# Optimization experiments

Hardware: AMD Instinct MI355X
Metric: run time of the kernel (lower is better)

Reference implementation:

```python
import jax, jax.numpy as jnp
import numpy as np
from jax import lax

B, C, H, W, K = 32, 128, 56, 56, 5
CR = C // 4          # reduced channels in weight-gen MLP
CE = 4 * C           # expanded channels
EPS = 1e-6


def setup_inputs() -> dict:
    key = jax.random.key(0)
    ks = jax.random.split(key, 8)
    s = lambda fan: 1.0 / np.sqrt(fan)
    return {
        "x": jax.random.normal(ks[0], (B, C, H, W), jnp.float32),
        "w_fc1": jax.random.normal(ks[1], (CR, C), jnp.float32) * s(C),
        "ln1_w": jnp.ones((CR,), jnp.float32),
        "ln1_b": jnp.zeros((CR,), jnp.float32),
        "w_fc2": jax.random.normal(ks[2], (C * K * K, CR), jnp.float32) * s(CR),
        "ln2_w": jnp.ones((C,), jnp.float32),
        "ln2_b": jnp.zeros((C,), jnp.float32),
        "w_expand": jax.random.normal(ks[3], (CE, C), jnp.float32) * s(C),
        "w_shrink": jax.random.normal(ks[4], (C, CE), jnp.float32) * s(CE),
        "grn_gamma": jax.random.normal(ks[5], (CE,), jnp.float32) * 0.1,
        "grn_beta": jax.random.normal(ks[6], (CE,), jnp.float32) * 0.1,
    }


def _ln(v, w, b, axis):
    u = v.mean(axis, keepdims=True)
    s2 = jnp.square(v - u).mean(axis, keepdims=True)
    return (v - u) * lax.rsqrt(s2 + EPS) * w + b


def reference(x, w_fc1, ln1_w, ln1_b, w_fc2, ln2_w, ln2_b, w_expand, w_shrink,
              grn_gamma, grn_beta):
    b, c, h, w = x.shape
    # ---- dynamic weight generation: pool -> fc1 -> LN -> fc2 ----
    pooled = x.mean((2, 3))                                  # [B, C]
    hdn = pooled @ w_fc1.T                                   # [B, CR]
    hdn = _ln(hdn, ln1_w, ln1_b, axis=-1)                    # channels_first LN over CR
    dyn = hdn @ w_fc2.T                                      # [B, C*K*K]
    dyn_w = dyn.reshape(b * c, 1, K, K)                      # per-sample depthwise kernels
    # ---- per-sample dynamic depthwise conv (groups = B*C) ----
    pad = K // 2
    out = lax.conv_general_dilated(
        x.reshape(1, b * c, h, w), dyn_w,
        window_strides=(1, 1), padding=[(pad, pad), (pad, pad)],
        dimension_numbers=("NCHW", "OIHW", "NCHW"),
        feature_group_count=b * c,
    ).reshape(b, c, h, w)
    # ---- LN (channels_first) over channel dim ----
    u = out.mean(1, keepdims=True)
    s2 = jnp.square(out - u).mean(1, keepdims=True)
    out = (out - u) * lax.rsqrt(s2 + EPS)
    out = ln2_w[None, :, None, None] * out + ln2_b[None, :, None, None]
    # ---- expand 1x1 -> GELU -> GRN -> shrink 1x1 ----
    out = jnp.einsum("bchw,oc->bohw", out, w_expand)         # [B, 4C, H, W]
    out = jax.nn.gelu(out, approximate=False)
    gx = jnp.sqrt(jnp.sum(jnp.square(out), axis=(2, 3), keepdims=True))  # [B,4C,1,1]
    nx = gx / (gx.mean(1, keepdims=True) + EPS)
    g = grn_gamma[None, :, None, None]
    bt = grn_beta[None, :, None, None]
    out = g * (out * nx) + bt + out
    out = jnp.einsum("bohw,co->bchw", out, w_shrink)         # [B, C, H, W]
    return out + x
```

## Files before the change

kernel.cpp:

```cpp
#include <hip/hip_runtime.h>
#include <hip/hip_bf16.h>

#define B_   32
#define C_   128
#define H_   56
#define W_   56
#define HW_  (H_*W_)
#define BHW_ (B_*HW_)
#define K5_  5
#define KK_  25
#define CR_  32
#define CE_  512
#define EPS_ 1e-6f

typedef __hip_bfloat16 bf16;
typedef __attribute__((ext_vector_type(8))) short short8;
typedef __attribute__((ext_vector_type(4))) float f32x4;


__device__ __forceinline__ float wave_reduce_sum(float v) {
#pragma unroll
  for (int off = 32; off > 0; off >>= 1) v += __shfl_down(v, off, 64);
  return v;
}
__device__ __forceinline__ float bf2f(unsigned short u) {
  return __uint_as_float(((unsigned)u) << 16);
}
__device__ __forceinline__ unsigned short f2bf_bits(float f) {
  bf16 h = __float2bfloat16(f);
  unsigned short u;
  __builtin_memcpy(&u, &h, 2);
  return u;
}
__device__ __forceinline__ float fast_gelu(float v) {
  float t = __expf(-1.702f * v);
  return v * __builtin_amdgcn_rcpf(1.0f + t);
}

__global__ __launch_bounds__(256) void prep_kernel(const float* __restrict__ we,
                                                   const float* __restrict__ ws,
                                                   bf16* __restrict__ weB,
                                                   bf16* __restrict__ wsB) {
  int i = blockIdx.x * 256 + threadIdx.x;
  if (i < CE_ * C_) {
    weB[i] = __float2bfloat16(we[i]);
    wsB[i] = __float2bfloat16(ws[i]);
  }
}

__global__ __launch_bounds__(256) void pool_kernel(const float* __restrict__ x,
                                                   float* __restrict__ pooled) {
  int bc = blockIdx.x;
  const float* xp = x + (size_t)bc * HW_;
  float s = 0.f;
  for (int i = threadIdx.x; i < HW_; i += 256) s += xp[i];
  s = wave_reduce_sum(s);
  __shared__ float red[4];
  int lane = threadIdx.x & 63, wid = threadIdx.x >> 6;
  if (lane == 0) red[wid] = s;
  __syncthreads();
  if (threadIdx.x == 0) pooled[bc] = (red[0] + red[1] + red[2] + red[3]) * (1.0f / HW_);
}

__global__ __launch_bounds__(256) void fc_kernel(const float* __restrict__ pooled,
                                                 const float* __restrict__ w_fc1,
                                                 const float* __restrict__ ln1_w,
                                                 const float* __restrict__ ln1_b,
                                                 const float* __restrict__ w_fc2,
                                                 float* __restrict__ dyn) {
  int b = blockIdx.x;
  int tid = threadIdx.x;
  __shared__ float sp[C_];
  __shared__ float sh[CR_];
  __shared__ float shn[CR_];
  __shared__ float stats[2];
  if (tid < C_) sp[tid] = pooled[b * C_ + tid];
  __syncthreads();
  if (tid < CR_) {
    float acc = 0.f;
    const float* wr = w_fc1 + tid * C_;
#pragma unroll 4
    for (int c = 0; c < C_; ++c) acc += sp[c] * wr[c];
    sh[tid] = acc;
  }
  __syncthreads();
  if (tid == 0) {
    float u = 0.f;
    for (int j = 0; j < CR_; ++j) u += sh[j];
    u *= (1.0f / CR_);
    float v = 0.f;
    for (int j = 0; j < CR_; ++j) { float d = sh[j] - u; v += d * d; }
    v *= (1.0f / CR_);
    stats[0] = u;
    stats[1] = rsqrtf(v + EPS_);
  }
  __syncthreads();
  if (tid < CR_) shn[tid] = (sh[tid] - stats[0]) * stats[1] * ln1_w[tid] + ln1_b[tid];
  __syncthreads();
  for (int i = tid; i < C_ * KK_; i += 256) {
    const float* wr = w_fc2 + i * CR_;
    float acc = 0.f;
#pragma unroll
    for (int j = 0; j < CR_; ++j) acc += shn[j] * wr[j];
    dyn[b * (C_ * KK_) + i] = acc;
  }
}

__global__ __launch_bounds__(256) void conv_kernel(const float* __restrict__ x,
                                                   const float* __restrict__ dyn,
                                                   bf16* __restrict__ z) {
  int bc = blockIdx.x;
  int b = bc >> 7;
  int c = bc & 127;
  int tid = threadIdx.x;
  __shared__ float xs[H_ * 64];
  __shared__ float wks[KK_];
  if (tid < H_ * 4) {
    int r = tid >> 2, q = tid & 3;
    int col = (q < 2) ? q : (56 + q);
    xs[r * 64 + col] = 0.f;
  }
  if (tid < KK_) wks[tid] = dyn[b * (C_ * KK_) + c * KK_ + tid];
  const float4* xp4 = reinterpret_cast<const float4*>(x + (size_t)bc * HW_);
  for (int i = tid; i < 784; i += 256) {
    float4 v = xp4[i];
    int h = i / 14, w4 = (i % 14) * 4;
    float* dst = &xs[h * 64 + 2 + w4];
    dst[0] = v.x; dst[1] = v.y; dst[2] = v.z; dst[3] = v.w;
  }
  __syncthreads();
  float wr[KK_];
#pragma unroll
  for (int j = 0; j < KK_; ++j) wr[j] = wks[j];
  for (int g = tid; g < 784; g += 256) {
    int h = g / 14;
    int w4 = (g % 14) * 4;
    float a0 = 0.f, a1 = 0.f, a2 = 0.f, a3 = 0.f;
#pragma unroll
    for (int dh = 0; dh < K5_; ++dh) {
      int hh = h + dh - 2;
      if (hh < 0 || hh >= H_) continue;
      const float* row = &xs[hh * 64 + w4];
      float4 va = *reinterpret_cast<const float4*>(row);
      float4 vb = *reinterpret_cast<const float4*>(row + 4);
      float v0 = va.x, v1 = va.y, v2 = va.z, v3 = va.w;
      float v4 = vb.x, v5 = vb.y, v6 = vb.z, v7 = vb.w;
      float u0 = wr[dh * 5 + 0], u1 = wr[dh * 5 + 1], u2 = wr[dh * 5 + 2];
      float u3 = wr[dh * 5 + 3], u4 = wr[dh * 5 + 4];
      a0 += v0 * u0 + v1 * u1 + v2 * u2 + v3 * u3 + v4 * u4;
      a1 += v1 * u0 + v2 * u1 + v3 * u2 + v4 * u3 + v5 * u4;
      a2 += v2 * u0 + v3 * u1 + v4 * u2 + v5 * u3 + v6 * u4;
      a3 += v3 * u0 + v4 * u1 + v5 * u2 + v6 * u3 + v7 * u4;
    }
    size_t base = (size_t)bc * HW_ + h * W_ + w4;
    ushort4 pk = make_ushort4(f2bf_bits(a0), f2bf_bits(a1), f2bf_bits(a2), f2bf_bits(a3));
    *reinterpret_cast<ushort4*>(reinterpret_cast<unsigned short*>(z) + base) = pk;
  }
}

__global__ __launch_bounds__(256) void ln_kernel(const bf16* __restrict__ z,
                                                 const float* __restrict__ ln2_w,
                                                 const float* __restrict__ ln2_b,
                                                 bf16* __restrict__ yT) {
  int hw0 = blockIdx.x * 64;
  int b = blockIdx.y;
  int tid = threadIdx.x;
  int wq = tid & 63;
  int cq = tid >> 6;
  __shared__ unsigned short zt[C_][64];
  __shared__ float redS[4][64];
  __shared__ float redQ[4][64];
  __shared__ float meanArr[64];
  __shared__ float invArr[64];
  float s = 0.f, q = 0.f;
  const unsigned short* zp = reinterpret_cast<const unsigned short*>(z);
#pragma unroll 4
  for (int k = 0; k < 32; ++k) {
    int c = cq * 32 + k;
    unsigned short u = zp[((size_t)(b * C_ + c)) * HW_ + hw0 + wq];
    float v = bf2f(u);
    s += v;
    q += v * v;
    zt[c][wq] = u;
  }
  redS[cq][wq] = s;
  redQ[cq][wq] = q;
  __syncthreads();
  if (cq == 0) {
    float ss = redS[0][wq] + redS[1][wq] + redS[2][wq] + redS[3][wq];
    float qq = redQ[0][wq] + redQ[1][wq] + redQ[2][wq] + redQ[3][wq];
    float m = ss * (1.0f / C_);
    float var = qq * (1.0f / C_) - m * m;
    meanArr[wq] = m;
    invArr[wq] = rsqrtf(fmaxf(var, 0.f) + EPS_);
  }
  __syncthreads();
  float m = meanArr[wq], iv = invArr[wq];
  unsigned short* yp =
      reinterpret_cast<unsigned short*>(yT) + ((size_t)(b * HW_ + hw0 + wq)) * C_ + cq * 32;
#pragma unroll
  for (int g = 0; g < 4; ++g) {
    unsigned short pk[8];
#pragma unroll
    for (int i = 0; i < 8; ++i) {
      int c = cq * 32 + g * 8 + i;
      float v = bf2f(zt[c][wq]);
      pk[i] = f2bf_bits((v - m) * iv * ln2_w[c] + ln2_b[c]);
    }
    int4 t;
    __builtin_memcpy(&t, pk, 16);
    *reinterpret_cast<int4*>(yp + g * 8) = t;
  }
}

__global__ __launch_bounds__(256, 4) void expand_mfma(const bf16* __restrict__ yT,
                                                      const bf16* __restrict__ weB,
                                                      bf16* __restrict__ eT,
                                                      float* __restrict__ gx2) {
  int j0 = blockIdx.x * 128;
  int o0 = blockIdx.y * 128;
  int tid = threadIdx.x;
  int lane = tid & 63, wid = tid >> 6;
  int wm = wid >> 1, wn = wid & 1;
  int quad = lane >> 4, l15 = lane & 15;
  __shared__ short As[128][40];
  __shared__ short Bs[128][40];
  f32x4 acc[4][4] = {};
  const short* yTs = reinterpret_cast<const short*>(yT);
  const short* weS = reinterpret_cast<const short*>(weB);
  for (int k0 = 0; k0 < C_; k0 += 32) {
#pragma unroll
    for (int t = tid; t < 512; t += 256) {
      int r = t >> 2, ch = t & 3;
      int4 va = *reinterpret_cast<const int4*>(yTs + (size_t)(j0 + r) * C_ + k0 + ch * 8);
      *reinterpret_cast<int4*>(&As[r][ch * 8]) = va;
      int4 vb = *reinterpret_cast<const int4*>(weS + (size_t)(o0 + r) * C_ + k0 + ch * 8);
      *reinterpret_cast<int4*>(&Bs[r][ch * 8]) = vb;
    }
    __syncthreads();
    short8 a[4], bfr[4];
#pragma unroll
    for (int mf = 0; mf < 4; ++mf)
      a[mf] = *reinterpret_cast<const short8*>(&As[wm * 64 + mf * 16 + l15][quad * 8]);
#pragma unroll
    for (int nf = 0; nf < 4; ++nf)
      bfr[nf] = *reinterpret_cast<const short8*>(&Bs[wn * 64 + nf * 16 + l15][quad * 8]);
#pragma unroll
    for (int mf = 0; mf < 4; ++mf)
#pragma unroll
      for (int nf = 0; nf < 4; ++nf)
        acc[mf][nf] = __builtin_amdgcn_mfma_f32_16x16x32_bf16(a[mf], bfr[nf], acc[mf][nf], 0, 0, 0);
    __syncthreads();
  }
  unsigned short* eP = reinterpret_cast<unsigned short*>(eT);
#pragma unroll
  for (int mf = 0; mf < 4; ++mf) {
    int jm = j0 + wm * 64 + mf * 16;
    int bb = jm / HW_;
    int jb = jm + quad * 4;
#pragma unroll
    for (int nf = 0; nf < 4; ++nf) {
      int o = o0 + wn * 64 + nf * 16 + l15;
      float g2 = 0.f;
#pragma unroll
      for (int r = 0; r < 4; ++r) {
        float ge = fast_gelu(acc[mf][nf][r]);
        g2 += ge * ge;
        eP[(size_t)(jb + r) * CE_ + o] = f2bf_bits(ge);
      }
      g2 += __shfl_xor(g2, 16, 64);
      g2 += __shfl_xor(g2, 32, 64);
      if (quad == 0) atomicAdd(&gx2[bb * CE_ + o], g2);
    }
  }
}

__global__ __launch_bounds__(512) void grn_scale_kernel(const float* __restrict__ gx2,
                                                        const float* __restrict__ gamma,
                                                        float* __restrict__ scale) {
  int b = blockIdx.x;
  int o = threadIdx.x;
  float gx = sqrtf(gx2[b * CE_ + o]);
  float s = wave_reduce_sum(gx);
  __shared__ float red[8];
  __shared__ float meansh;
  int lane = o & 63, wid = o >> 6;
  if (lane == 0) red[wid] = s;
  __syncthreads();
  if (o == 0) {
    float t = 0.f;
    for (int i = 0; i < 8; ++i) t += red[i];
    meansh = t * (1.0f / CE_);
  }
  __syncthreads();
  scale[b * CE_ + o] = 1.0f + gamma[o] * (gx / (meansh + EPS_));
}

__global__ __launch_bounds__(128) void sb_kernel(const float* __restrict__ w_shrink,
                                                 const float* __restrict__ beta,
                                                 float* __restrict__ sb) {
  int c = threadIdx.x;
  float acc = 0.f;
  for (int o = 0; o < CE_; ++o) acc += w_shrink[c * CE_ + o] * beta[o];
  sb[c] = acc;
}

__global__ __launch_bounds__(256) void scale_ws_kernel(const float* __restrict__ ws,
                                                       const float* __restrict__ scale,
                                                       bf16* __restrict__ sws) {
  int c = blockIdx.x;
  int b = blockIdx.y;
  const float* sp = scale + b * CE_;
  const float* wp = ws + (size_t)c * CE_;
  bf16* op = sws + ((size_t)(b * C_ + c)) * CE_;
  for (int i = threadIdx.x; i < CE_; i += 256)
    op[i] = __float2bfloat16(wp[i] * sp[i]);
}

__global__ __launch_bounds__(256, 4) void shrink_mfma(const bf16* __restrict__ eT,
                                                      const bf16* __restrict__ sws,
                                                      const float* __restrict__ sb,
                                                      const float* __restrict__ x,
                                                      float* __restrict__ out) {
  int hw0 = blockIdx.x * 128;
  int b = blockIdx.y;
  int tid = threadIdx.x;
  int lane = tid & 63, wid = tid >> 6;
  int wm = wid >> 1, wn = wid & 1;
  int quad = lane >> 4, l15 = lane & 15;
  __shared__ short As[128][40];
  __shared__ short Bs[128][40];
  f32x4 acc[4][4] = {};
  const short* eS = reinterpret_cast<const short*>(eT) + (size_t)b * HW_ * CE_;
  const short* wsS = reinterpret_cast<const short*>(sws) + (size_t)b * C_ * CE_;
  for (int k0 = 0; k0 < CE_; k0 += 32) {
#pragma unroll
    for (int t = tid; t < 512; t += 256) {
      int r = t >> 2, ch = t & 3;
      int hwc = hw0 + r; if (hwc >= HW_) hwc = HW_ - 1;
      int4 va = *reinterpret_cast<const int4*>(eS + (size_t)hwc * CE_ + k0 + ch * 8);
      *reinterpret_cast<int4*>(&As[r][ch * 8]) = va;
      int4 vb = *reinterpret_cast<const int4*>(wsS + (size_t)r * CE_ + k0 + ch * 8);
      *reinterpret_cast<int4*>(&Bs[r][ch * 8]) = vb;
    }
    __syncthreads();
    short8 a[4], bfr[4];
#pragma unroll
    for (int mf = 0; mf < 4; ++mf)
      a[mf] = *reinterpret_cast<const short8*>(&As[wm * 64 + mf * 16 + l15][quad * 8]);
#pragma unroll
    for (int nf = 0; nf < 4; ++nf)
      bfr[nf] = *reinterpret_cast<const short8*>(&Bs[wn * 64 + nf * 16 + l15][quad * 8]);
#pragma unroll
    for (int mf = 0; mf < 4; ++mf)
#pragma unroll
      for (int nf = 0; nf < 4; ++nf)
        acc[mf][nf] = __builtin_amdgcn_mfma_f32_16x16x32_bf16(a[mf], bfr[nf], acc[mf][nf], 0, 0, 0);
    __syncthreads();
  }
#pragma unroll
  for (int mf = 0; mf < 4; ++mf) {
    int hw = hw0 + wm * 64 + mf * 16 + quad * 4;
    if (hw >= HW_) continue;
#pragma unroll
    for (int nf = 0; nf < 4; ++nf) {
      int c = wn * 64 + nf * 16 + l15;
      size_t base = ((size_t)(b * C_ + c)) * HW_ + hw;
      float add = sb[c];
      float4 xv = *reinterpret_cast<const float4*>(x + base);
      float4 ov;
      ov.x = acc[mf][nf][0] + add + xv.x;
      ov.y = acc[mf][nf][1] + add + xv.y;
      ov.z = acc[mf][nf][2] + add + xv.z;
      ov.w = acc[mf][nf][3] + add + xv.w;
      *reinterpret_cast<float4*>(out + base) = ov;
    }
  }
}

extern "C" void kernel_launch(void* const* d_in, const int* in_sizes, int n_in,
                              void* d_out, int out_size, void* d_ws, size_t ws_size,
                              hipStream_t stream) {
  (void)in_sizes; (void)n_in; (void)out_size; (void)ws_size;
  const float* x        = (const float*)d_in[0];
  const float* w_fc1    = (const float*)d_in[1];
  const float* ln1_w    = (const float*)d_in[2];
  const float* ln1_b    = (const float*)d_in[3];
  const float* w_fc2    = (const float*)d_in[4];
  const float* ln2_w    = (const float*)d_in[5];
  const float* ln2_b    = (const float*)d_in[6];
  const float* w_expand = (const float*)d_in[7];
  const float* w_shrink = (const float*)d_in[8];
  const float* gamma    = (const float*)d_in[9];
  const float* beta     = (const float*)d_in[10];
  float* out = (float*)d_out;

  char* ws = (char*)d_ws;
  float* pooled = (float*)(ws + 0);
  float* dyn    = (float*)(ws + 16384);
  float* gx2    = (float*)(ws + 425984);
  float* scale  = (float*)(ws + 491520);
  float* sb     = (float*)(ws + 557056);
  bf16*  weB    = (bf16*)(ws + 557568);
  bf16*  wsB    = (bf16*)(ws + 688640);
  bf16*  yT     = (bf16*)(ws + 819712);
  bf16*  sws    = (bf16*)(ws + 819712);
  bf16*  eT     = (bf16*)(ws + 26509824);
  bf16*  z      = eT;
  (void)wsB;

  prep_kernel<<<256, 256, 0, stream>>>(w_expand, w_shrink, weB, wsB);
  pool_kernel<<<B_ * C_, 256, 0, stream>>>(x, pooled);
  fc_kernel<<<B_, 256, 0, stream>>>(pooled, w_fc1, ln1_w, ln1_b, w_fc2, dyn);
  conv_kernel<<<B_ * C_, 256, 0, stream>>>(x, dyn, z);
  ln_kernel<<<dim3(49, B_), 256, 0, stream>>>(z, ln2_w, ln2_b, yT);
  hipMemsetAsync(gx2, 0, B_ * CE_ * sizeof(float), stream);
  expand_mfma<<<dim3(784, 4), 256, 0, stream>>>(yT, weB, eT, gx2);
  grn_scale_kernel<<<B_, 512, 0, stream>>>(gx2, gamma, scale);
  sb_kernel<<<1, 128, 0, stream>>>(w_shrink, beta, sb);
  scale_ws_kernel<<<dim3(C_, B_), 256, 0, stream>>>(w_shrink, scale, sws);
  shrink_mfma<<<dim3(25, B_), 256, 0, stream>>>(eT, sws, sb, x, out);
}
```

Measured before the change: 303.0 us.

## Stage GEMM and LN epilogues through LDS for coalesced stores; pad conv rows

The expand, shrink and LN kernels now write their outputs to shared memory first and then copy them to global memory as wide, coalesced 16-byte row stores. Before, each lane wrote scattered 2-byte or strided float4 values. The conv kernel pads two zero rows above and below the tile so the inner loop drops its row bounds checks, and the unused bf16 conversion of w_shrink is removed. The extra LDS round trips and barriers add latency and raise shared-memory use, which can lower occupancy, most visibly in expand_mfma where smem grows to about 34 KB.

After: 297.3 us. No clear change (-1.9%).

```diff
diff --git a/kernel.cpp b/kernel.cpp
--- a/kernel.cpp
+++ b/kernel.cpp
@@ -38,14 +38,9 @@
 }
 
 __global__ __launch_bounds__(256) void prep_kernel(const float* __restrict__ we,
-                                                   const float* __restrict__ ws,
-                                                   bf16* __restrict__ weB,
-                                                   bf16* __restrict__ wsB) {
+                                                   bf16* __restrict__ weB) {
   int i = blockIdx.x * 256 + threadIdx.x;
-  if (i < CE_ * C_) {
-    weB[i] = __float2bfloat16(we[i]);
-    wsB[i] = __float2bfloat16(ws[i]);
-  }
+  if (i < CE_ * C_) weB[i] = __float2bfloat16(we[i]);
 }
 
 __global__ __launch_bounds__(256) void pool_kernel(const float* __restrict__ x,
@@ -113,19 +108,24 @@
   int b = bc >> 7;
   int c = bc & 127;
   int tid = threadIdx.x;
-  __shared__ float xs[H_ * 64];
+  __shared__ float xs[(H_ + 4) * 64];
   __shared__ float wks[KK_];
-  if (tid < H_ * 4) {
+  {
+    int r = tid >> 6;
+    int rr = (r < 2) ? r : (56 + r);
+    xs[rr * 64 + (tid & 63)] = 0.f;
+  }
+  if (tid < 224) {
     int r = tid >> 2, q = tid & 3;
     int col = (q < 2) ? q : (56 + q);
-    xs[r * 64 + col] = 0.f;
+    xs[(r + 2) * 64 + col] = 0.f;
   }
   if (tid < KK_) wks[tid] = dyn[b * (C_ * KK_) + c * KK_ + tid];
   const float4* xp4 = reinterpret_cast<const float4*>(x + (size_t)bc * HW_);
   for (int i = tid; i < 784; i += 256) {
     float4 v = xp4[i];
     int h = i / 14, w4 = (i % 14) * 4;
-    float* dst = &xs[h * 64 + 2 + w4];
+    float* dst = &xs[(h + 2) * 64 + 2 + w4];
     dst[0] = v.x; dst[1] = v.y; dst[2] = v.z; dst[3] = v.w;
   }
   __syncthreads();
@@ -138,9 +138,7 @@
     float a0 = 0.f, a1 = 0.f, a2 = 0.f, a3 = 0.f;
 #pragma unroll
     for (int dh = 0; dh < K5_; ++dh) {
-      int hh = h + dh - 2;
-      if (hh < 0 || hh >= H_) continue;
-      const float* row = &xs[hh * 64 + w4];
+      const float* row = &xs[(h + dh) * 64 + w4];
       float4 va = *reinterpret_cast<const float4*>(row);
       float4 vb = *reinterpret_cast<const float4*>(row + 4);
       float v0 = va.x, v1 = va.y, v2 = va.z, v3 = va.w;
@@ -168,6 +166,7 @@
   int wq = tid & 63;
   int cq = tid >> 6;
   __shared__ unsigned short zt[C_][64];
+  __shared__ unsigned short yt[64][136];
   __shared__ float redS[4][64];
   __shared__ float redQ[4][64];
   __shared__ float meanArr[64];
@@ -196,8 +195,6 @@
   }
   __syncthreads();
   float m = meanArr[wq], iv = invArr[wq];
-  unsigned short* yp =
-      reinterpret_cast<unsigned short*>(yT) + ((size_t)(b * HW_ + hw0 + wq)) * C_ + cq * 32;
 #pragma unroll
   for (int g = 0; g < 4; ++g) {
     unsigned short pk[8];
@@ -209,7 +206,16 @@
     }
     int4 t;
     __builtin_memcpy(&t, pk, 16);
-    *reinterpret_cast<int4*>(yp + g * 8) = t;
+    *reinterpret_cast<int4*>(&yt[wq][cq * 32 + g * 8]) = t;
+  }
+  __syncthreads();
+  unsigned short* yp = reinterpret_cast<unsigned short*>(yT);
+#pragma unroll
+  for (int i = 0; i < 4; ++i) {
+    int t = tid + 256 * i;
+    int row = t >> 4, ch = t & 15;
+    int4 v = *reinterpret_cast<const int4*>(&yt[row][ch * 8]);
+    *reinterpret_cast<int4*>(yp + ((size_t)(b * HW_ + hw0 + row)) * C_ + ch * 8) = v;
   }
 }
 
@@ -223,8 +229,9 @@
   int lane = tid & 63, wid = tid >> 6;
   int wm = wid >> 1, wn = wid & 1;
   int quad = lane >> 4, l15 = lane & 15;
-  __shared__ short As[128][40];
-  __shared__ short Bs[128][40];
+  __shared__ __align__(16) char smem[128 * 136 * 2];
+  short (*As)[40] = reinterpret_cast<short(*)[40]>(&smem[0]);
+  short (*Bs)[40] = reinterpret_cast<short(*)[40]>(&smem[10240]);
   f32x4 acc[4][4] = {};
   const short* yTs = reinterpret_cast<const short*>(yT);
   const short* weS = reinterpret_cast<const short*>(weB);
@@ -252,26 +259,35 @@
         acc[mf][nf] = __builtin_amdgcn_mfma_f32_16x16x32_bf16(a[mf], bfr[nf], acc[mf][nf], 0, 0, 0);
     __syncthreads();
   }
-  unsigned short* eP = reinterpret_cast<unsigned short*>(eT);
+  short (*Es)[136] = reinterpret_cast<short(*)[136]>(&smem[0]);
 #pragma unroll
   for (int mf = 0; mf < 4; ++mf) {
     int jm = j0 + wm * 64 + mf * 16;
     int bb = jm / HW_;
-    int jb = jm + quad * 4;
+    int jrow = wm * 64 + mf * 16 + quad * 4;
 #pragma unroll
     for (int nf = 0; nf < 4; ++nf) {
-      int o = o0 + wn * 64 + nf * 16 + l15;
+      int oc = wn * 64 + nf * 16 + l15;
       float g2 = 0.f;
 #pragma unroll
       for (int r = 0; r < 4; ++r) {
         float ge = fast_gelu(acc[mf][nf][r]);
         g2 += ge * ge;
-        eP[(size_t)(jb + r) * CE_ + o] = f2bf_bits(ge);
+        Es[jrow + r][oc] = (short)f2bf_bits(ge);
       }
       g2 += __shfl_xor(g2, 16, 64);
       g2 += __shfl_xor(g2, 32, 64);
-      if (quad == 0) atomicAdd(&gx2[bb * CE_ + o], g2);
-    }
+      if (quad == 0) atomicAdd(&gx2[bb * CE_ + o0 + oc], g2);
+    }
+  }
+  __syncthreads();
+  unsigned short* eP = reinterpret_cast<unsigned short*>(eT);
+#pragma unroll
+  for (int i = 0; i < 8; ++i) {
+    int t = tid + 256 * i;
+    int row = t >> 4, ch = t & 15;
+    int4 v = *reinterpret_cast<const int4*>(&Es[row][ch * 8]);
+    *reinterpret_cast<int4*>(eP + (size_t)(j0 + row) * CE_ + o0 + ch * 8) = v;
   }
 }
 
@@ -328,8 +344,9 @@
   int lane = tid & 63, wid = tid >> 6;
   int wm = wid >> 1, wn = wid & 1;
   int quad = lane >> 4, l15 = lane & 15;
-  __shared__ short As[128][40];
-  __shared__ short Bs[128][40];
+  __shared__ __align__(16) char smem[64 * 136 * 4];
+  short (*As)[40] = reinterpret_cast<short(*)[40]>(&smem[0]);
+  short (*Bs)[40] = reinterpret_cast<short(*)[40]>(&smem[10240]);
   f32x4 acc[4][4] = {};
   const short* eS = reinterpret_cast<const short*>(eT) + (size_t)b * HW_ * CE_;
   const short* wsS = reinterpret_cast<const short*>(sws) + (size_t)b * C_ * CE_;
@@ -358,23 +375,41 @@
         acc[mf][nf] = __builtin_amdgcn_mfma_f32_16x16x32_bf16(a[mf], bfr[nf], acc[mf][nf], 0, 0, 0);
     __syncthreads();
   }
-#pragma unroll
-  for (int mf = 0; mf < 4; ++mf) {
-    int hw = hw0 + wm * 64 + mf * 16 + quad * 4;
-    if (hw >= HW_) continue;
-#pragma unroll
-    for (int nf = 0; nf < 4; ++nf) {
-      int c = wn * 64 + nf * 16 + l15;
-      size_t base = ((size_t)(b * C_ + c)) * HW_ + hw;
-      float add = sb[c];
-      float4 xv = *reinterpret_cast<const float4*>(x + base);
-      float4 ov;
-      ov.x = acc[mf][nf][0] + add + xv.x;
-      ov.y = acc[mf][nf][1] + add + xv.y;
-      ov.z = acc[mf][nf][2] + add + xv.z;
-      ov.w = acc[mf][nf][3] + add + xv.w;
-      *reinterpret_cast<float4*>(out + base) = ov;
-    }
+  float (*Ef)[136] = reinterpret_cast<float(*)[136]>(&smem[0]);
+#pragma unroll
+  for (int phase = 0; phase < 2; ++phase) {
+    if (wn == phase) {
+#pragma unroll
+      for (int mf = 0; mf < 4; ++mf) {
+        int hwr = wm * 64 + mf * 16 + quad * 4;
+#pragma unroll
+        for (int nf = 0; nf < 4; ++nf) {
+          int cr = nf * 16 + l15;
+          *reinterpret_cast<f32x4*>(&Ef[cr][hwr]) = acc[mf][nf];
+        }
+      }
+    }
+    __syncthreads();
+#pragma unroll
+    for (int i = 0; i < 8; ++i) {
+      int t = tid + 256 * i;
+      int row = t >> 5, ch = t & 31;
+      int hw = hw0 + ch * 4;
+      if (hw < HW_) {
+        int c = phase * 64 + row;
+        size_t base = ((size_t)(b * C_ + c)) * HW_ + hw;
+        float add = sb[c];
+        f32x4 av = *reinterpret_cast<const f32x4*>(&Ef[row][ch * 4]);
+        float4 xv = *reinterpret_cast<const float4*>(x + base);
+        float4 ov;
+        ov.x = av.x + add + xv.x;
+        ov.y = av.y + add + xv.y;
+        ov.z = av.z + add + xv.z;
+        ov.w = av.w + add + xv.w;
+        *reinterpret_cast<float4*>(out + base) = ov;
+      }
+    }
+    __syncthreads();
   }
 }
 
@@ -402,14 +437,12 @@
   float* scale  = (float*)(ws + 491520);
   float* sb     = (float*)(ws + 557056);
   bf16*  weB    = (bf16*)(ws + 557568);
-  bf16*  wsB    = (bf16*)(ws + 688640);
   bf16*  yT     = (bf16*)(ws + 819712);
   bf16*  sws    = (bf16*)(ws + 819712);
   bf16*  eT     = (bf16*)(ws + 26509824);
   bf16*  z      = eT;
-  (void)wsB;
-
-  prep_kernel<<<256, 256, 0, stream>>>(w_expand, w_shrink, weB, wsB);
+
+  prep_kernel<<<256, 256, 0, stream>>>(w_expand, weB);
   pool_kernel<<<B_ * C_, 256, 0, stream>>>(x, pooled);
   fc_kernel<<<B_, 256, 0, stream>>>(pooled, w_fc1, ln1_w, ln1_b, w_fc2, dyn);
   conv_kernel<<<B_ * C_, 256, 0, stream>>>(x, dyn, z);
```
